# Optimization experiments

Measured on AMD Instinct MI355X. Metric: run time of the kernel, lower is better.

## Reference

```python
import jax, jax.numpy as jnp
import numpy as np
from jax import lax

N, L, V, ES, HS = 16384, 512, 32000, 32, 64


def setup_inputs() -> dict:
    key = jax.random.key(0)
    k_tok, k_len, k_emb, k_wih, k_whh, k_bih, k_bhh = jax.random.split(key, 7)
    # valid tokens in [1, V) so that (x != 0).sum(1) == true prefix length
    tok = jax.random.randint(k_tok, (N, L), 1, V)
    lengths = jax.random.randint(k_len, (N,), 0, L + 1)  # includes empty seqs
    x = jnp.where(jnp.arange(L)[None, :] < lengths[:, None], tok, 0)
    s = 0.1
    embedding = jax.random.normal(k_emb, (V, ES), dtype=jnp.float32) * s
    w_ih = jax.random.normal(k_wih, (3 * HS, ES), dtype=jnp.float32) * s  # [r|z|n] stacked (torch order)
    w_hh = jax.random.normal(k_whh, (3 * HS, HS), dtype=jnp.float32) * s
    b_ih = jax.random.normal(k_bih, (3 * HS,), dtype=jnp.float32) * s
    b_hh = jax.random.normal(k_bhh, (3 * HS,), dtype=jnp.float32) * s
    return {"x": x, "embedding": embedding, "w_ih": w_ih, "w_hh": w_hh,
            "b_ih": b_ih, "b_hh": b_hh}


def reference(x, embedding, w_ih, w_hh, b_ih, b_hh):
    # Faithful math: final GRU hidden state over the nonzero prefix of each row;
    # rows with length 0 return zeros (h0). Equivalent to bucketed
    # pack_padded_sequence + GRU + scatter of final hidden states.
    n, l = x.shape
    hs = w_hh.shape[1]
    lengths = (x != 0).sum(axis=1)  # [n]

    def step(h, inp):
        t, xt = inp                      # xt: [n] token ids at time t
        e = embedding[xt]                # [n, es] gather
        gx = e @ w_ih.T + b_ih           # [n, 3*hs]
        gh = h @ w_hh.T + b_hh           # [n, 3*hs]
        xr, xz, xn = jnp.split(gx, 3, axis=-1)
        hr, hz, hn = jnp.split(gh, 3, axis=-1)
        r = jax.nn.sigmoid(xr + hr)
        z = jax.nn.sigmoid(xz + hz)
        ng = jnp.tanh(xn + r * hn)
        h_new = (1.0 - z) * ng + z * h   # torch GRU update
        h = jnp.where((t < lengths)[:, None], h_new, h)  # freeze past length
        return h, None

    h0 = jnp.zeros((n, hs), dtype=embedding.dtype)
    hT, _ = lax.scan(step, h0, (jnp.arange(l), x.T))
    return hT
```

## Files before the change

### kernel.cpp

```cpp
#include <hip/hip_runtime.h>

#define N_SEQ 16384
#define LSEQ  512
#define VOCAB 32000
#define ES    32
#define HS    64
#define LDH   72
#define TS    18

#define SC_RZ (-1.4426950408889634f)
#define SC_N  (-2.8853900817779268f)

typedef _Float16 v8h __attribute__((ext_vector_type(8)));
typedef float    v4f __attribute__((ext_vector_type(4)));

#define NLB (N_SEQ / 256)
#define NEB (VOCAB * ES / 256)
__global__ __launch_bounds__(256) void k_prep(const int* __restrict__ x,
                                              const float* __restrict__ emb,
                                              const float* __restrict__ whh,
                                              const float* __restrict__ wih,
                                              int* __restrict__ len,
                                              int* __restrict__ hist,
                                              _Float16* __restrict__ ef,
                                              _Float16* __restrict__ wpk,
                                              _Float16* __restrict__ wpe){
  int b = blockIdx.x;
  if (b < NLB){
    int row = b * 256 + threadIdx.x;
    const int* xr = x + (size_t)row * LSEQ;
    int lo = 0, hi = LSEQ;
    while (lo < hi){ int mid = (lo + hi) >> 1; if (xr[mid] != 0) lo = mid + 1; else hi = mid; }
    len[row] = lo;
    atomicAdd(&hist[lo], 1);
  } else if (b < NLB + NEB){
    int i = (b - NLB) * 256 + threadIdx.x;
    ef[i] = (_Float16)emb[i];
  } else if (b < NLB + NEB + 6){
    int tid = (b - NLB - NEB) * 256 + threadIdx.x;
    int f = tid >> 6, l = tid & 63;
    int jt = f >> 1, kf = f & 1;
    float sc = (jt < 8) ? SC_RZ : SC_N;
    #pragma unroll
    for (int i = 0; i < 8; ++i){
      int row = jt * 16 + (l & 15);
      int col = kf * 32 + (l >> 4) * 8 + i;
      wpk[(size_t)tid * 8 + i] = (_Float16)(sc * whh[row * HS + col]);
    }
  } else {
    int tid = (b - NLB - NEB - 6) * 256 + threadIdx.x;
    int tile = tid >> 6, l = tid & 63;
    float sc = ((tile >> 2) < 2) ? SC_RZ : SC_N;
    #pragma unroll
    for (int i = 0; i < 8; ++i){
      int row = tile * 16 + (l & 15);
      int col = (l >> 4) * 8 + i;
      wpe[(size_t)tid * 8 + i] = (_Float16)(sc * wih[row * ES + col]);
    }
  }
}

__global__ __launch_bounds__(1024) void k_scatter(const int* __restrict__ hist,
                                                  const int* __restrict__ len,
                                                  int* __restrict__ gcnt,
                                                  int* __restrict__ perm){
  __shared__ int buf[1024];
  __shared__ int offs[513];
  int i = threadIdx.x;
  buf[i] = (i < 513) ? hist[i] : 0;
  __syncthreads();
  for (int d = 1; d < 1024; d <<= 1){
    int v = (i >= d) ? buf[i - d] : 0;
    __syncthreads();
    buf[i] += v;
    __syncthreads();
  }
  if (i < 513) offs[i] = (i == 0) ? 0 : buf[i - 1];
  __syncthreads();
  int s = blockIdx.x * 1024 + i;
  int l = len[s];
  int pos = offs[l] + atomicAdd(&gcnt[l], 1);
  perm[pos] = s;
}

__global__ __launch_bounds__(256, 4) void k_gru(
    const int* __restrict__ x, const _Float16* __restrict__ ef,
    const _Float16* __restrict__ wpk, const _Float16* __restrict__ wpe,
    const float* __restrict__ bih, const float* __restrict__ bhh,
    const int* __restrict__ perm, const int* __restrict__ len,
    float* __restrict__ out)
{
  __shared__ __align__(16) _Float16 hb[2][16 * LDH];
  __shared__ unsigned short tok[(LSEQ + 2) * TS];
  int qt   = threadIdx.x >> 6;
  int w = blockIdx.x >> 8, cq = blockIdx.x & 255;
  int rank = w * 256 + ((w & 1) ? (255 - cq) : cq);
  int grp  = 1023 - rank;
  int lane = threadIdx.x & 63;
  int q = lane >> 4, c = lane & 15;
  int uu = qt*16 + c;

  v8h bfh[3][2], bfe[3];
  #pragma unroll
  for (int g = 0; g < 3; ++g){
    int tile = g*4 + qt;
    #pragma unroll
    for (int kf = 0; kf < 2; ++kf)
      bfh[g][kf] = *(const v8h*)(wpk + ((size_t)(tile*2 + kf)*64 + lane)*8);
    bfe[g] = *(const v8h*)(wpe + ((size_t)tile*64 + lane)*8);
  }

  int sq[4], ln[4];
  #pragma unroll
  for (int r = 0; r < 4; ++r){
    int s = perm[grp * 16 + q*4 + r];
    sq[r] = s;
    ln[r] = len[s];
  }
  float br  = SC_RZ * (bih[uu]      + bhh[uu]);
  float bz  = SC_RZ * (bih[HS + uu] + bhh[HS + uu]);
  float ben = SC_N  *  bih[2*HS + uu];
  float bhn = SC_N  *  bhh[2*HS + uu];
  v4f brq  = {br, br, br, br};
  v4f bzq  = {bz, bz, bz, bz};
  v4f benq = {ben, ben, ben, ben};
  v4f bhnq = {bhn, bhn, bhn, bhn};

  float h[4];
  #pragma unroll
  for (int r = 0; r < 4; ++r) h[r] = 0.f;

  for (int i = threadIdx.x; i < 16*LDH; i += 256) hb[0][i] = (_Float16)0.f;

  for (int j = threadIdx.x; j < 16*LSEQ; j += 256){
    int s = j >> 9, tt = j & (LSEQ-1);
    tok[tt*TS + s] = (unsigned short)x[(size_t)perm[grp*16 + s] * LSEQ + tt];
  }
  if (threadIdx.x < 32){
    tok[(LSEQ + (threadIdx.x >> 4))*TS + (threadIdx.x & 15)] = 0;
  }
  __syncthreads();

  int tmax = max(max(ln[0], ln[1]), max(ln[2], ln[3]));
  tmax = max(tmax, __shfl_xor(tmax, 16, 64));
  tmax = max(tmax, __shfl_xor(tmax, 32, 64));
  int tmin = min(min(ln[0], ln[1]), min(ln[2], ln[3]));
  tmin = min(tmin, __shfl_xor(tmin, 16, 64));
  tmin = min(tmin, __shfl_xor(tmin, 32, 64));

  v8h aec, aen;
  v4f pra, prb, pza, pzb, dea, deb;
  {
    int tk0 = tok[0*TS + c];
    aec = *(const v8h*)(ef + (size_t)tk0 * ES + q*8);
    pra = __builtin_amdgcn_mfma_f32_16x16x32_f16(aec, bfe[0], brq,  0,0,0);
    pza = __builtin_amdgcn_mfma_f32_16x16x32_f16(aec, bfe[1], bzq,  0,0,0);
    dea = __builtin_amdgcn_mfma_f32_16x16x32_f16(aec, bfe[2], benq, 0,0,0);
    int tk1 = tok[1*TS + c];
    aen = *(const v8h*)(ef + (size_t)tk1 * ES + q*8);
  }

  #define GRU_STEP(FREEZE, ACONS, ALOAD, PRR, PRZ, DEN, PRRn, PRZn, DENn, RB, WB) \
  {                                                                            \
    int tkn = tok[(t + 2)*TS + c];                                             \
    v8h a0 = *(const v8h*)(&hb[RB][c*LDH + q*8]);                              \
    v8h a1 = *(const v8h*)(&hb[RB][c*LDH + 32 + q*8]);                         \
    v4f zr  = __builtin_amdgcn_mfma_f32_16x16x32_f16(a1, bfh[0][1], PRR, 0,0,0);\
    v4f Dr  = __builtin_amdgcn_mfma_f32_16x16x32_f16(a0, bfh[0][0], zr,  0,0,0);\
    v4f zz  = __builtin_amdgcn_mfma_f32_16x16x32_f16(a1, bfh[1][1], PRZ, 0,0,0);\
    v4f Dz  = __builtin_amdgcn_mfma_f32_16x16x32_f16(a0, bfh[1][0], zz,  0,0,0);\
    v4f zh  = __builtin_amdgcn_mfma_f32_16x16x32_f16(a1, bfh[2][1], bhnq,0,0,0);\
    v4f Dhn = __builtin_amdgcn_mfma_f32_16x16x32_f16(a0, bfh[2][0], zh,  0,0,0);\
    _Pragma("unroll")                                                          \
    for (int r = 0; r < 4; ++r){                                               \
      float rg   = __builtin_amdgcn_rcpf(1.f + __builtin_amdgcn_exp2f(Dr[r])); \
      float zg   = __builtin_amdgcn_rcpf(1.f + __builtin_amdgcn_exp2f(Dz[r])); \
      float te   = __builtin_amdgcn_exp2f(DEN[r] + rg * Dhn[r]);               \
      float ng   = fmaf(2.f, __builtin_amdgcn_rcpf(1.f + te), -1.f);           \
      float hnew = ng + zg * (h[r] - ng);                                      \
      h[r]       = (FREEZE && t >= ln[r]) ? h[r] : hnew;                       \
    }                                                                          \
    PRRn = __builtin_amdgcn_mfma_f32_16x16x32_f16(ACONS, bfe[0], brq,  0,0,0); \
    PRZn = __builtin_amdgcn_mfma_f32_16x16x32_f16(ACONS, bfe[1], bzq,  0,0,0); \
    DENn = __builtin_amdgcn_mfma_f32_16x16x32_f16(ACONS, bfe[2], benq, 0,0,0); \
    ALOAD = *(const v8h*)(ef + (size_t)tkn * ES + q*8);           \
    _Pragma("unroll")                                                          \
    for (int r = 0; r < 4; ++r)                                                \
      hb[WB][(q*4 + r)*LDH + uu] = (_Float16)h[r];                             \
    asm volatile("s_waitcnt lgkmcnt(0)" ::: "memory");                         \
    __builtin_amdgcn_s_barrier();                                              \
    asm volatile("" ::: "memory");                                             \
  }

  int t = 0;
  for (; t + 1 < tmin; ){
    GRU_STEP(0, aen, aec, pra, pza, dea, prb, pzb, deb, 0, 1); ++t;
    GRU_STEP(0, aec, aen, prb, pzb, deb, pra, pza, dea, 1, 0); ++t;
  }
  for (; t + 1 < tmax; ){
    GRU_STEP(1, aen, aec, pra, pza, dea, prb, pzb, deb, 0, 1); ++t;
    GRU_STEP(1, aec, aen, prb, pzb, deb, pra, pza, dea, 1, 0); ++t;
  }
  if (t < tmax){
    GRU_STEP(1, aen, aec, pra, pza, dea, prb, pzb, deb, 0, 1); ++t;
  }
  #undef GRU_STEP

  #pragma unroll
  for (int r = 0; r < 4; ++r)
    out[(size_t)sq[r] * HS + uu] = h[r];
}

extern "C" void kernel_launch(void* const* d_in, const int* in_sizes, int n_in,
                              void* d_out, int out_size, void* d_ws, size_t ws_size,
                              hipStream_t stream){
  const int*   x   = (const int*)  d_in[0];
  const float* emb = (const float*)d_in[1];
  const float* wih = (const float*)d_in[2];
  const float* whh = (const float*)d_in[3];
  const float* bih = (const float*)d_in[4];
  const float* bhh = (const float*)d_in[5];
  float* out = (float*)d_out;

  char* ws = (char*)d_ws;
  size_t off = 0;
  _Float16* ef  = (_Float16*)(ws + off);  off += (size_t)VOCAB * ES * sizeof(_Float16);
  _Float16* wpk = (_Float16*)(ws + off);  off += (size_t)24 * 64 * 8 * sizeof(_Float16);
  _Float16* wpe = (_Float16*)(ws + off);  off += (size_t)12 * 64 * 8 * sizeof(_Float16);
  off = (off + 255) & ~(size_t)255;
  int* len  = (int*)(ws + off);           off += (size_t)N_SEQ * sizeof(int);
  int* perm = (int*)(ws + off);           off += (size_t)N_SEQ * sizeof(int);
  int* hist = (int*)(ws + off);           off += 513 * sizeof(int);
  int* gcnt = (int*)(ws + off);           off += 513 * sizeof(int);

  hipMemsetAsync(hist, 0, 2 * 513 * sizeof(int), stream);
  k_prep   <<<NLB + NEB + 9, 256, 0, stream>>>(x, emb, whh, wih, len, hist, ef, wpk, wpe);
  k_scatter<<<N_SEQ / 1024, 1024, 0, stream>>>(hist, len, gcnt, perm);
  k_gru    <<<N_SEQ / 16,    256, 0, stream>>>(x, ef, wpk, wpe, bih, bhh, perm, len, out);
}
```

Before: 309.9 us.

## Merge GRU gate math into one reciprocal and regroup prep kernels

The per-element GRU update is rewritten so the z-gate sigmoid and the tanh-based candidate share a single reciprocal. The remaining arithmetic is expressed as packed two-wide float ops, which cuts transcendental instructions on the serial recurrence path. The prep work is also regrouped: the length search runs alone, and the scan/scatter, a vectorized embedding fp16 conversion, and the weight packing share one launch. This shortens the critical dependency chain per timestep at some cost in rounding behaviour near saturation.

```diff
diff --git a/kernel.cpp b/kernel.cpp
--- a/kernel.cpp
+++ b/kernel.cpp
@@ -13,74 +13,84 @@
 
 typedef _Float16 v8h __attribute__((ext_vector_type(8)));
 typedef float    v4f __attribute__((ext_vector_type(4)));
-
-#define NLB (N_SEQ / 256)
-#define NEB (VOCAB * ES / 256)
-__global__ __launch_bounds__(256) void k_prep(const int* __restrict__ x,
+typedef float    v2f __attribute__((ext_vector_type(2)));
+
+__global__ __launch_bounds__(256) void k_len(const int* __restrict__ x,
+                                             int* __restrict__ len,
+                                             int* __restrict__ hist){
+  int row = blockIdx.x * 256 + threadIdx.x;
+  const int* xr = x + (size_t)row * LSEQ;
+  int lo = 0, hi = LSEQ;
+  while (lo < hi){ int mid = (lo + hi) >> 1; if (xr[mid] != 0) lo = mid + 1; else hi = mid; }
+  len[row] = lo;
+  atomicAdd(&hist[lo], 1);
+}
+
+#define SCB   16
+#define EMBV  125
+__global__ __launch_bounds__(1024) void k_mid(const int* __restrict__ hist,
+                                              const int* __restrict__ len,
+                                              int* __restrict__ gcnt,
+                                              int* __restrict__ perm,
                                               const float* __restrict__ emb,
                                               const float* __restrict__ whh,
                                               const float* __restrict__ wih,
-                                              int* __restrict__ len,
-                                              int* __restrict__ hist,
                                               _Float16* __restrict__ ef,
                                               _Float16* __restrict__ wpk,
                                               _Float16* __restrict__ wpe){
   int b = blockIdx.x;
-  if (b < NLB){
-    int row = b * 256 + threadIdx.x;
-    const int* xr = x + (size_t)row * LSEQ;
-    int lo = 0, hi = LSEQ;
-    while (lo < hi){ int mid = (lo + hi) >> 1; if (xr[mid] != 0) lo = mid + 1; else hi = mid; }
-    len[row] = lo;
-    atomicAdd(&hist[lo], 1);
-  } else if (b < NLB + NEB){
-    int i = (b - NLB) * 256 + threadIdx.x;
-    ef[i] = (_Float16)emb[i];
-  } else if (b < NLB + NEB + 6){
-    int tid = (b - NLB - NEB) * 256 + threadIdx.x;
-    int f = tid >> 6, l = tid & 63;
-    int jt = f >> 1, kf = f & 1;
-    float sc = (jt < 8) ? SC_RZ : SC_N;
-    #pragma unroll
-    for (int i = 0; i < 8; ++i){
-      int row = jt * 16 + (l & 15);
-      int col = kf * 32 + (l >> 4) * 8 + i;
-      wpk[(size_t)tid * 8 + i] = (_Float16)(sc * whh[row * HS + col]);
+  if (b < SCB){
+    __shared__ int buf[1024];
+    __shared__ int offs[513];
+    int i = threadIdx.x;
+    buf[i] = (i < 513) ? hist[i] : 0;
+    __syncthreads();
+    for (int d = 1; d < 1024; d <<= 1){
+      int v = (i >= d) ? buf[i - d] : 0;
+      __syncthreads();
+      buf[i] += v;
+      __syncthreads();
     }
+    if (i < 513) offs[i] = (i == 0) ? 0 : buf[i - 1];
+    __syncthreads();
+    int s = b * 1024 + i;
+    int l = len[s];
+    int pos = offs[l] + atomicAdd(&gcnt[l], 1);
+    perm[pos] = s;
+  } else if (b < SCB + EMBV){
+    int i = ((b - SCB) * 1024 + threadIdx.x) * 8;
+    float4 f0 = *(const float4*)(emb + i);
+    float4 f1 = *(const float4*)(emb + i + 4);
+    v8h o;
+    o[0] = (_Float16)f0.x; o[1] = (_Float16)f0.y;
+    o[2] = (_Float16)f0.z; o[3] = (_Float16)f0.w;
+    o[4] = (_Float16)f1.x; o[5] = (_Float16)f1.y;
+    o[6] = (_Float16)f1.z; o[7] = (_Float16)f1.w;
+    *(v8h*)(ef + i) = o;
   } else {
-    int tid = (b - NLB - NEB - 6) * 256 + threadIdx.x;
-    int tile = tid >> 6, l = tid & 63;
-    float sc = ((tile >> 2) < 2) ? SC_RZ : SC_N;
-    #pragma unroll
-    for (int i = 0; i < 8; ++i){
-      int row = tile * 16 + (l & 15);
-      int col = (l >> 4) * 8 + i;
-      wpe[(size_t)tid * 8 + i] = (_Float16)(sc * wih[row * ES + col]);
+    int tid = (b - SCB - EMBV) * 1024 + threadIdx.x;
+    if (tid < 1536){
+      int f = tid >> 6, l = tid & 63;
+      int jt = f >> 1, kf = f & 1;
+      float sc = (jt < 8) ? SC_RZ : SC_N;
+      #pragma unroll
+      for (int i = 0; i < 8; ++i){
+        int row = jt * 16 + (l & 15);
+        int col = kf * 32 + (l >> 4) * 8 + i;
+        wpk[(size_t)tid * 8 + i] = (_Float16)(sc * whh[row * HS + col]);
+      }
+    } else if (tid < 1536 + 768){
+      int t2 = tid - 1536;
+      int tile = t2 >> 6, l = t2 & 63;
+      float sc = ((tile >> 2) < 2) ? SC_RZ : SC_N;
+      #pragma unroll
+      for (int i = 0; i < 8; ++i){
+        int row = tile * 16 + (l & 15);
+        int col = (l >> 4) * 8 + i;
+        wpe[(size_t)t2 * 8 + i] = (_Float16)(sc * wih[row * ES + col]);
+      }
     }
   }
-}
-
-__global__ __launch_bounds__(1024) void k_scatter(const int* __restrict__ hist,
-                                                  const int* __restrict__ len,
-                                                  int* __restrict__ gcnt,
-                                                  int* __restrict__ perm){
-  __shared__ int buf[1024];
-  __shared__ int offs[513];
-  int i = threadIdx.x;
-  buf[i] = (i < 513) ? hist[i] : 0;
-  __syncthreads();
-  for (int d = 1; d < 1024; d <<= 1){
-    int v = (i >= d) ? buf[i - d] : 0;
-    __syncthreads();
-    buf[i] += v;
-    __syncthreads();
-  }
-  if (i < 513) offs[i] = (i == 0) ? 0 : buf[i - 1];
-  __syncthreads();
-  int s = blockIdx.x * 1024 + i;
-  int l = len[s];
-  int pos = offs[l] + atomicAdd(&gcnt[l], 1);
-  perm[pos] = s;
 }
 
 __global__ __launch_bounds__(256, 4) void k_gru(
@@ -160,6 +170,8 @@
     aen = *(const v8h*)(ef + (size_t)tk1 * ES + q*8);
   }
 
+  const v2f one2 = {1.f, 1.f};
+
   #define GRU_STEP(FREEZE, ACONS, ALOAD, PRR, PRZ, DEN, PRRn, PRZn, DENn, RB, WB) \
   {                                                                            \
     int tkn = tok[(t + 2)*TS + c];                                             \
@@ -172,13 +184,33 @@
     v4f zh  = __builtin_amdgcn_mfma_f32_16x16x32_f16(a1, bfh[2][1], bhnq,0,0,0);\
     v4f Dhn = __builtin_amdgcn_mfma_f32_16x16x32_f16(a0, bfh[2][0], zh,  0,0,0);\
     _Pragma("unroll")                                                          \
-    for (int r = 0; r < 4; ++r){                                               \
-      float rg   = __builtin_amdgcn_rcpf(1.f + __builtin_amdgcn_exp2f(Dr[r])); \
-      float zg   = __builtin_amdgcn_rcpf(1.f + __builtin_amdgcn_exp2f(Dz[r])); \
-      float te   = __builtin_amdgcn_exp2f(DEN[r] + rg * Dhn[r]);               \
-      float ng   = fmaf(2.f, __builtin_amdgcn_rcpf(1.f + te), -1.f);           \
-      float hnew = ng + zg * (h[r] - ng);                                      \
-      h[r]       = (FREEZE && t >= ln[r]) ? h[r] : hnew;                       \
+    for (int p = 0; p < 2; ++p){                                               \
+      v2f dr = {Dr[2*p],  Dr[2*p+1]};                                          \
+      v2f dz = {Dz[2*p],  Dz[2*p+1]};                                          \
+      v2f dn = {Dhn[2*p], Dhn[2*p+1]};                                         \
+      v2f de = {DEN[2*p], DEN[2*p+1]};                                         \
+      v2f hh = {h[2*p],   h[2*p+1]};                                           \
+      v2f er, ez, rg, te, rd;                                                  \
+      er[0] = __builtin_amdgcn_exp2f(dr[0]);                                   \
+      er[1] = __builtin_amdgcn_exp2f(dr[1]);                                   \
+      ez[0] = __builtin_amdgcn_exp2f(dz[0]);                                   \
+      ez[1] = __builtin_amdgcn_exp2f(dz[1]);                                   \
+      v2f ar = er + one2;                                                      \
+      rg[0] = __builtin_amdgcn_rcpf(ar[0]);                                    \
+      rg[1] = __builtin_amdgcn_rcpf(ar[1]);                                    \
+      v2f ta = de + rg * dn;                                                   \
+      te[0] = __builtin_amdgcn_exp2f(ta[0]);                                   \
+      te[1] = __builtin_amdgcn_exp2f(ta[1]);                                   \
+      v2f A   = te + one2;                                                     \
+      v2f hp1 = hh + one2;                                                     \
+      v2f e2  = ez + ez;                                                       \
+      v2f num = A * hp1 + e2;                                                  \
+      v2f den = A * (ez + one2);                                               \
+      rd[0] = __builtin_amdgcn_rcpf(den[0]);                                   \
+      rd[1] = __builtin_amdgcn_rcpf(den[1]);                                   \
+      v2f hn2 = num * rd - one2;                                               \
+      h[2*p]   = (FREEZE && t >= ln[2*p])   ? h[2*p]   : hn2[0];               \
+      h[2*p+1] = (FREEZE && t >= ln[2*p+1]) ? h[2*p+1] : hn2[1];               \
     }                                                                          \
     PRRn = __builtin_amdgcn_mfma_f32_16x16x32_f16(ACONS, bfe[0], brq,  0,0,0); \
     PRZn = __builtin_amdgcn_mfma_f32_16x16x32_f16(ACONS, bfe[1], bzq,  0,0,0); \
@@ -234,7 +266,8 @@
   int* gcnt = (int*)(ws + off);           off += 513 * sizeof(int);
 
   hipMemsetAsync(hist, 0, 2 * 513 * sizeof(int), stream);
-  k_prep   <<<NLB + NEB + 9, 256, 0, stream>>>(x, emb, whh, wih, len, hist, ef, wpk, wpe);
-  k_scatter<<<N_SEQ / 1024, 1024, 0, stream>>>(hist, len, gcnt, perm);
-  k_gru    <<<N_SEQ / 16,    256, 0, stream>>>(x, ef, wpk, wpe, bih, bhh, perm, len, out);
-}
+  k_len <<<N_SEQ / 256, 256, 0, stream>>>(x, len, hist);
+  k_mid <<<SCB + EMBV + 3, 1024, 0, stream>>>(hist, len, gcnt, perm,
+                                              emb, whh, wih, ef, wpk, wpe);
+  k_gru <<<N_SEQ / 16,    256, 0, stream>>>(x, ef, wpk, wpe, bih, bhh, perm, len, out);
+}
```

Measured after the change: 311.6 us. About the same (+0.6%).
